# Kernel optimization log

Measured on AMD Instinct MI355X. Metric: run time of the kernel, lower is better.

Reference implementation:

```python
import jax, jax.numpy as jnp
import numpy as np

VOCAB, D_MODEL, N_EXPERTS, TOP_K = 32000, 768, 8, 2
D_FF = 4 * D_MODEL
BATCH, SEQ = 2, 2048


def setup_inputs() -> dict:
    key = jax.random.key(0)
    ks = jax.random.split(key, 6)
    s = 0.02
    return {
        "x": jax.random.randint(ks[0], (BATCH, SEQ), 0, VOCAB),
        "emb": jax.random.normal(ks[1], (VOCAB, D_MODEL), jnp.float32) * s,
        "gate_w": jax.random.normal(ks[2], (D_MODEL, N_EXPERTS), jnp.float32) * s,
        "gate_b": jnp.zeros((N_EXPERTS,), jnp.float32),
        "exp_w": jax.random.normal(ks[3], (N_EXPERTS, D_MODEL, D_FF), jnp.float32) * s,
        "exp_b": jnp.zeros((N_EXPERTS, D_FF), jnp.float32),
        "head_w": jax.random.normal(ks[4], (D_FF, VOCAB), jnp.float32) * s,
        "head_b": jnp.zeros((VOCAB,), jnp.float32),
    }


def reference(x, emb, gate_w, gate_b, exp_w, exp_b, head_w, head_b):
    B, S = x.shape
    h = emb[x]                                   # [B,S,D] embedding gather
    t = h.reshape(B * S, -1)                     # [T,D] token view
    logits = t @ gate_w + gate_b                 # [T,E] router
    topv, topi = jax.lax.top_k(logits, TOP_K)    # top-2 routing
    w = jax.nn.softmax(topv, axis=-1)            # renormalized gate weights
    T = t.shape[0]
    gates = jnp.zeros_like(logits).at[jnp.arange(T)[:, None], topi].set(w)  # [T,E]
    # expert FFN: Linear(d_model -> 4*d_model) + ReLU, dense over experts
    exp_out = jax.nn.relu(jnp.einsum('td,edf->tef', t, exp_w) + exp_b)      # [T,E,F]
    moe = jnp.einsum('te,tef->tf', gates, exp_out)                          # combine
    out = moe @ head_w + head_b                  # [T,V]
    return out.reshape(B, S, -1)
```

## Files before the change

### kernel.cpp

```cpp
#include <hip/hip_runtime.h>

typedef unsigned short u16;
typedef __attribute__((ext_vector_type(8))) short short8;
typedef __attribute__((ext_vector_type(4))) float f32x4;

#define T_TOKENS 4096
#define DMODEL   768
#define DFF      3072
#define NEXP     8
#define NVOCAB   32000

__device__ __forceinline__ u16 f2bf(float f) {
  unsigned u = __float_as_uint(f);
  u += 0x7FFFu + ((u >> 16) & 1u);
  return (u16)(u >> 16);
}
__device__ __forceinline__ float bf2f(u16 b) {
  return __uint_as_float(((unsigned)b) << 16);
}

__device__ __forceinline__ void async_load16(const void* g, void* lds) {
  __builtin_amdgcn_global_load_lds((const __attribute__((address_space(1))) void*)g,
                                   (__attribute__((address_space(3))) void*)lds, 16, 0, 0);
}

#define SBAR() __builtin_amdgcn_s_barrier()
#define VMCNT(n) asm volatile("s_waitcnt vmcnt(" #n ")")

__global__ __launch_bounds__(256) void k_embed_router(
    const int* __restrict__ x, const float* __restrict__ emb,
    const float* __restrict__ gw, const float* __restrict__ gb,
    u16* __restrict__ tbf, int* __restrict__ counts,
    int* __restrict__ tlist, float* __restrict__ wlist)
{
  __shared__ float partial[4][NEXP];
  const int t = blockIdx.x;
  const int tok = x[t];
  const float* er = emb + (size_t)tok * DMODEL;
  float p[NEXP];
#pragma unroll
  for (int e = 0; e < NEXP; ++e) p[e] = 0.f;
#pragma unroll
  for (int i = 0; i < 3; ++i) {
    const int d = threadIdx.x + i * 256;
    const float v = er[d];
    tbf[(size_t)t * DMODEL + d] = f2bf(v);
#pragma unroll
    for (int e = 0; e < NEXP; ++e) p[e] += v * gw[d * NEXP + e];
  }
#pragma unroll
  for (int e = 0; e < NEXP; ++e)
#pragma unroll
    for (int m = 32; m >= 1; m >>= 1) p[e] += __shfl_xor(p[e], m);
  const int lane = threadIdx.x & 63, wv = threadIdx.x >> 6;
  if (lane == 0)
    for (int e = 0; e < NEXP; ++e) partial[wv][e] = p[e];
  __syncthreads();
  if (threadIdx.x == 0) {
    float l[NEXP];
    for (int e = 0; e < NEXP; ++e)
      l[e] = partial[0][e] + partial[1][e] + partial[2][e] + partial[3][e] + gb[e];
    int i0 = 0;
    for (int e = 1; e < NEXP; ++e) if (l[e] > l[i0]) i0 = e;
    int i1 = -1;
    for (int e = 0; e < NEXP; ++e) { if (e == i0) continue; if (i1 < 0 || l[e] > l[i1]) i1 = e; }
    const float w0 = 1.f / (1.f + expf(l[i1] - l[i0]));
    int p0 = atomicAdd(&counts[0 * NEXP + i0], 1);
    tlist[(0 * NEXP + i0) * T_TOKENS + p0] = t;
    wlist[(0 * NEXP + i0) * T_TOKENS + p0] = w0;
    int p1 = atomicAdd(&counts[1 * NEXP + i1], 1);
    tlist[(1 * NEXP + i1) * T_TOKENS + p1] = t;
    wlist[(1 * NEXP + i1) * T_TOKENS + p1] = 1.f - w0;
  }
}

__global__ __launch_bounds__(256) void k_transpose_cvt(
    const float* __restrict__ src, u16* __restrict__ dst, int R, int C)
{
  __shared__ float tile[32][33];
  const float* s = src + (size_t)blockIdx.z * R * C;
  u16* d = dst + (size_t)blockIdx.z * R * C;
  const int tx = threadIdx.x & 31, ty = threadIdx.x >> 5;
  const int c = blockIdx.x * 32 + tx;
#pragma unroll
  for (int i = 0; i < 4; ++i) {
    const int r = blockIdx.y * 32 + ty + i * 8;
    tile[ty + i * 8][tx] = s[(size_t)r * C + c];
  }
  __syncthreads();
  const int rr = blockIdx.y * 32 + tx;
#pragma unroll
  for (int i = 0; i < 4; ++i) {
    const int cc = blockIdx.x * 32 + ty + i * 8;
    d[(size_t)cc * R + rr] = f2bf(tile[tx][ty + i * 8]);
  }
}

template <int SLOT1>
__global__ __launch_bounds__(256) void k_ffn_slot(
    const u16* __restrict__ tbf, const u16* __restrict__ BT,
    const float* __restrict__ eb, const int* __restrict__ counts,
    const int* __restrict__ tlist, const float* __restrict__ wlist,
    u16* __restrict__ moe)
{
  const int e = blockIdx.z;
  const int cnt = counts[SLOT1 * NEXP + e];
  const int mb = blockIdx.y;
  if (mb * 128 >= cnt) return;
  const int base = (SLOT1 * NEXP + e) * T_TOKENS + mb * 128;
  const int lim = cnt - mb * 128;

  __shared__ u16 aT[128 * 64];
  __shared__ u16 bT[128 * 64];
  const int tid = threadIdx.x;
  const int wave = tid >> 6, lane = tid & 63;
  const int wm = wave >> 1, wn = wave & 1;
  const int kg = lane >> 4, fr = lane & 15;
  const int n0 = blockIdx.x * 128;
  const u16* Be = BT + (size_t)e * DFF * DMODEL;

  int tokm[4];
#pragma unroll
  for (int it = 0; it < 4; ++it) {
    const int m = (it * 256 + tid) >> 3;
    tokm[it] = tlist[base + (m < lim ? m : lim - 1)];
  }

  f32x4 acc[4][4] = {};
  for (int ks = 0; ks < DMODEL / 64; ++ks) {
    __syncthreads();
    const int kb = ks * 64;
#pragma unroll
    for (int it = 0; it < 4; ++it) {
      const int c = it * 256 + tid;
      const int m = c >> 3;
      const int slot = (c & 7) ^ (m & 7);
      async_load16(tbf + (size_t)tokm[it] * DMODEL + kb + slot * 8,
                   &aT[(it * 256 + wave * 64) * 8]);
      async_load16(Be + (size_t)(n0 + m) * DMODEL + kb + slot * 8,
                   &bT[(it * 256 + wave * 64) * 8]);
    }
    __syncthreads();
#pragma unroll
    for (int kk = 0; kk < 2; ++kk) {
      short8 af[4], bf[4];
#pragma unroll
      for (int i = 0; i < 4; ++i) {
        const int am = wm * 64 + i * 16 + fr;
        const int kc = kk * 4 + kg;
        af[i] = *(const short8*)&aT[(am * 8 + (kc ^ (am & 7))) * 8];
        const int bn = wn * 64 + i * 16 + fr;
        bf[i] = *(const short8*)&bT[(bn * 8 + (kc ^ (bn & 7))) * 8];
      }
#pragma unroll
      for (int i = 0; i < 4; ++i)
#pragma unroll
        for (int j = 0; j < 4; ++j)
          acc[i][j] = __builtin_amdgcn_mfma_f32_16x16x32_bf16(af[i], bf[j], acc[i][j], 0, 0, 0);
    }
  }

  int trow[4][4]; float wrow[4][4];
#pragma unroll
  for (int i = 0; i < 4; ++i)
#pragma unroll
    for (int r = 0; r < 4; ++r) {
      const int row = wm * 64 + i * 16 + kg * 4 + r;
      if (row < lim) { trow[i][r] = tlist[base + row]; wrow[i][r] = wlist[base + row]; }
      else trow[i][r] = -1;
    }
#pragma unroll
  for (int j = 0; j < 4; ++j) {
    const int col = n0 + wn * 64 + j * 16 + fr;
    const float b = eb[e * DFF + col];
#pragma unroll
    for (int i = 0; i < 4; ++i)
#pragma unroll
      for (int r = 0; r < 4; ++r) {
        if (trow[i][r] < 0) continue;
        float v = acc[i][j][r] + b;
        v = v > 0.f ? v : 0.f;
        v *= wrow[i][r];
        u16* dst = &moe[(size_t)trow[i][r] * DFF + col];
        if (SLOT1) v += bf2f(*dst);
        *dst = f2bf(v);
      }
  }
}

__device__ __forceinline__ short8 frag(const u16* buf, int row, int kc) {
  return *(const short8*)(buf + (row * 8 + (kc ^ (row & 7))) * 8);
}

__global__ __launch_bounds__(512, 2) void k_head(
    const u16* __restrict__ A, const u16* __restrict__ BT,
    const float* __restrict__ bias, float* __restrict__ C)
{
  __shared__ u16 aL[2][256 * 64];
  __shared__ u16 bL[2][256 * 64];
  const int tid = threadIdx.x;
  const int lane = tid & 63, wave = tid >> 6;
  const int wm = wave >> 2, wn = wave & 3;
  const int kg = lane >> 4, fr = lane & 15;
  const int wg = (int)blockIdx.x;
  const int swz = (wg & 7) * 250 + (wg >> 3);
  const int m0 = (swz & 15) * 256;
  const int n0 = (swz >> 4) * 256;
  const int K = DFF, NT = K / 64;

  size_t gAo[2], gBo[2]; int lAo[2], lBo[2];
#pragma unroll
  for (int i = 0; i < 2; ++i) {
    const int c = i * 512 + tid, rl = c >> 3, s = c & 7;
    const int rA = (rl & 63) + ((rl >> 6) << 7);
    const int gsA = s ^ (rA & 7);
    gAo[i] = (size_t)(m0 + rA) * K + gsA * 8;
    lAo[i] = rA * 64 + s * 8;
    const int rB = (rl & 31) + ((rl >> 5) << 6);
    const int gsB = s ^ (rB & 7);
    gBo[i] = (size_t)(n0 + rB) * K + gsB * 8;
    lBo[i] = rB * 64 + s * 8;
  }
  auto stageA = [&](int kb, u16* buf, int h) {
#pragma unroll
    for (int i = 0; i < 2; ++i)
      async_load16(A + gAo[i] + (size_t)(h * 64) * K + kb, buf + lAo[i] + h * 4096);
  };
  auto stageB = [&](int kb, u16* buf, int h) {
#pragma unroll
    for (int i = 0; i < 2; ++i)
      async_load16(BT + gBo[i] + (size_t)(h * 32) * K + kb, buf + lBo[i] + h * 2048);
  };

  f32x4 acc[8][4] = {};
  short8 af0[4][2], af1[4][2], bfl[2][2], bfh[2][2];

  stageA(0, aL[0], 0); stageA(0, aL[0], 1);
  stageB(0, bL[0], 0); stageB(0, bL[0], 1);
  stageA(64, aL[1], 0); stageB(64, bL[1], 0); stageA(64, aL[1], 1);
  VMCNT(6);
  __builtin_amdgcn_sched_barrier(0);
  SBAR();
#pragma unroll
  for (int mi = 0; mi < 4; ++mi)
#pragma unroll
    for (int kk = 0; kk < 2; ++kk)
      af0[mi][kk] = frag(aL[0], wm * 128 + mi * 16 + fr, kk * 4 + kg);
#pragma unroll
  for (int ni = 0; ni < 2; ++ni)
#pragma unroll
    for (int kk = 0; kk < 2; ++kk)
      bfl[ni][kk] = frag(bL[0], wn * 64 + ni * 16 + fr, kk * 4 + kg);

  for (int t = 0; t < NT; ++t) {
    const int cur = t & 1;
    const u16* a_ = aL[cur];
    const u16* b_ = bL[cur];
    u16* aw = aL[cur];
    u16* bw = bL[cur];
    const u16* an = aL[cur ^ 1];
    const u16* bn = bL[cur ^ 1];
    const int kb1 = (t + 1) * 64, kb2 = (t + 2) * 64;

#pragma unroll
    for (int ni = 0; ni < 2; ++ni)
#pragma unroll
      for (int kk = 0; kk < 2; ++kk)
        bfh[ni][kk] = frag(b_, wn * 64 + 32 + ni * 16 + fr, kk * 4 + kg);
    if (t + 1 < NT) stageB(kb1, bL[cur ^ 1], 1);
    __builtin_amdgcn_s_setprio(1);
#pragma unroll
    for (int mi = 0; mi < 4; ++mi)
#pragma unroll
      for (int ni = 0; ni < 2; ++ni)
#pragma unroll
        for (int kk = 0; kk < 2; ++kk)
          acc[mi][ni] = __builtin_amdgcn_mfma_f32_16x16x32_bf16(af0[mi][kk], bfl[ni][kk], acc[mi][ni], 0, 0, 0);
    __builtin_amdgcn_s_setprio(0);
    SBAR();

#pragma unroll
    for (int mi = 0; mi < 4; ++mi)
#pragma unroll
      for (int kk = 0; kk < 2; ++kk)
        af1[mi][kk] = frag(a_, wm * 128 + 64 + mi * 16 + fr, kk * 4 + kg);
    if (t + 2 < NT) stageA(kb2, aw, 0);
    __builtin_amdgcn_s_setprio(1);
#pragma unroll
    for (int mi = 0; mi < 4; ++mi)
#pragma unroll
      for (int ni = 0; ni < 2; ++ni)
#pragma unroll
        for (int kk = 0; kk < 2; ++kk)
          acc[mi][ni + 2] = __builtin_amdgcn_mfma_f32_16x16x32_bf16(af0[mi][kk], bfh[ni][kk], acc[mi][ni + 2], 0, 0, 0);
    __builtin_amdgcn_s_setprio(0);
    if (t < NT - 2) { VMCNT(8); } else if (t == NT - 2) { VMCNT(6); }
    __builtin_amdgcn_sched_barrier(0);
    SBAR();

    if (t + 1 < NT) {
#pragma unroll
      for (int mi = 0; mi < 4; ++mi)
#pragma unroll
        for (int kk = 0; kk < 2; ++kk)
          af0[mi][kk] = frag(an, wm * 128 + mi * 16 + fr, kk * 4 + kg);
    }
    if (t + 2 < NT) stageB(kb2, bw, 0);
    __builtin_amdgcn_s_setprio(1);
#pragma unroll
    for (int mi = 0; mi < 4; ++mi)
#pragma unroll
      for (int ni = 0; ni < 2; ++ni)
#pragma unroll
        for (int kk = 0; kk < 2; ++kk)
          acc[mi + 4][ni] = __builtin_amdgcn_mfma_f32_16x16x32_bf16(af1[mi][kk], bfl[ni][kk], acc[mi + 4][ni], 0, 0, 0);
    __builtin_amdgcn_s_setprio(0);
    if (t < NT - 2) { VMCNT(8); } else if (t == NT - 2) { VMCNT(4); }
    __builtin_amdgcn_sched_barrier(0);
    SBAR();

    if (t + 1 < NT) {
#pragma unroll
      for (int ni = 0; ni < 2; ++ni)
#pragma unroll
        for (int kk = 0; kk < 2; ++kk)
          bfl[ni][kk] = frag(bn, wn * 64 + ni * 16 + fr, kk * 4 + kg);
    }
    if (t + 2 < NT) stageA(kb2, aw, 1);
    __builtin_amdgcn_s_setprio(1);
#pragma unroll
    for (int mi = 0; mi < 4; ++mi)
#pragma unroll
      for (int ni = 0; ni < 2; ++ni)
#pragma unroll
        for (int kk = 0; kk < 2; ++kk)
          acc[mi + 4][ni + 2] = __builtin_amdgcn_mfma_f32_16x16x32_bf16(af1[mi][kk], bfh[ni][kk], acc[mi + 4][ni + 2], 0, 0, 0);
    __builtin_amdgcn_s_setprio(0);
    if (t < NT - 2) { VMCNT(6); } else if (t == NT - 2) { VMCNT(0); }
    __builtin_amdgcn_sched_barrier(0);
    SBAR();
  }

#pragma unroll
  for (int ni = 0; ni < 4; ++ni) {
    const int col = n0 + wn * 64 + ni * 16 + fr;
    const float b = bias[col];
#pragma unroll
    for (int mi = 0; mi < 8; ++mi) {
      const int row = m0 + wm * 128 + (mi >> 2) * 64 + (mi & 3) * 16 + kg * 4;
#pragma unroll
      for (int r = 0; r < 4; ++r)
        __builtin_nontemporal_store(acc[mi][ni][r] + b,
                                    &C[(size_t)(row + r) * NVOCAB + col]);
    }
  }
}

extern "C" void kernel_launch(void* const* d_in, const int* in_sizes, int n_in,
                              void* d_out, int out_size, void* d_ws, size_t ws_size,
                              hipStream_t stream) {
  const int*   x     = (const int*)d_in[0];
  const float* emb   = (const float*)d_in[1];
  const float* gw    = (const float*)d_in[2];
  const float* gb    = (const float*)d_in[3];
  const float* expw  = (const float*)d_in[4];
  const float* expb  = (const float*)d_in[5];
  const float* headw = (const float*)d_in[6];
  const float* headb = (const float*)d_in[7];
  float* out = (float*)d_out;

  char* ws = (char*)d_ws;
  size_t off = 0;
  auto alloc = [&](size_t bytes) { size_t r = off; off += (bytes + 255) & ~(size_t)255; return r; };
  u16*   tbf    = (u16*)(ws + alloc((size_t)T_TOKENS * DMODEL * 2));
  int*   counts = (int*)(ws + alloc(2 * NEXP * 4));
  int*   tlist  = (int*)(ws + alloc((size_t)2 * NEXP * T_TOKENS * 4));
  float* wlist  = (float*)(ws + alloc((size_t)2 * NEXP * T_TOKENS * 4));
  u16*   expwT  = (u16*)(ws + alloc((size_t)NEXP * DFF * DMODEL * 2));
  u16*   headwT = (u16*)(ws + alloc((size_t)NVOCAB * DFF * 2));
  u16*   moe    = (u16*)(ws + alloc((size_t)T_TOKENS * DFF * 2));

  hipMemsetAsync(counts, 0, 2 * NEXP * 4, stream);
  k_embed_router<<<T_TOKENS, 256, 0, stream>>>(x, emb, gw, gb, tbf, counts, tlist, wlist);
  k_transpose_cvt<<<dim3(DFF / 32, DMODEL / 32, NEXP), 256, 0, stream>>>(expw, expwT, DMODEL, DFF);
  k_transpose_cvt<<<dim3(NVOCAB / 32, DFF / 32, 1), 256, 0, stream>>>(headw, headwT, DFF, NVOCAB);
  k_ffn_slot<0><<<dim3(DFF / 128, T_TOKENS / 128, NEXP), 256, 0, stream>>>(
      tbf, expwT, expb, counts, tlist, wlist, moe);
  k_ffn_slot<1><<<dim3(DFF / 128, T_TOKENS / 128, NEXP), 256, 0, stream>>>(
      tbf, expwT, expb, counts, tlist, wlist, moe);
  k_head<<<(T_TOKENS / 256) * (NVOCAB / 256), 512, 0, stream>>>(moe, headwT, headb, out);
}
```

Measured before the change: 1.246 ms.

## Shrink head GEMM tile to 128x128 with 4 waves and re-pipeline LDS staging

The vocabulary head GEMM moves from 256x256 tiles with 8 waves and 512 threads to 128x128 tiles with 4 waves and 256 threads, each wave computing 64x64. The K-loop is restructured into four phases per 64-wide K step, with explicit lgkmcnt waits and new vmcnt thresholds. The grid grows fourfold, which aims to improve load balance and occupancy. In exchange, reuse of A and B tiles per loaded byte drops, so global and L2 traffic rises.

Result: slower. 1.883 ms (+51.2%).

```diff
diff --git a/kernel.cpp b/kernel.cpp
--- a/kernel.cpp
+++ b/kernel.cpp
@@ -26,6 +26,8 @@
 
 #define SBAR() __builtin_amdgcn_s_barrier()
 #define VMCNT(n) asm volatile("s_waitcnt vmcnt(" #n ")")
+#define LGKM(n)  asm volatile("s_waitcnt lgkmcnt(" #n ")")
+#define SCHEDB() __builtin_amdgcn_sched_barrier(0)
 
 __global__ __launch_bounds__(256) void k_embed_router(
     const int* __restrict__ x, const float* __restrict__ emb,
@@ -192,165 +194,147 @@
   return *(const short8*)(buf + (row * 8 + (kc ^ (row & 7))) * 8);
 }
 
-__global__ __launch_bounds__(512, 2) void k_head(
+__global__ __launch_bounds__(256) void k_head(
     const u16* __restrict__ A, const u16* __restrict__ BT,
     const float* __restrict__ bias, float* __restrict__ C)
 {
-  __shared__ u16 aL[2][256 * 64];
-  __shared__ u16 bL[2][256 * 64];
+  __shared__ u16 aL[2][128 * 64];
+  __shared__ u16 bL[2][128 * 64];
   const int tid = threadIdx.x;
   const int lane = tid & 63, wave = tid >> 6;
-  const int wm = wave >> 2, wn = wave & 3;
+  const int wm = wave >> 1, wn = wave & 1;
   const int kg = lane >> 4, fr = lane & 15;
   const int wg = (int)blockIdx.x;
-  const int swz = (wg & 7) * 250 + (wg >> 3);
-  const int m0 = (swz & 15) * 256;
-  const int n0 = (swz >> 4) * 256;
+  const int swz = (wg & 7) * 1000 + (wg >> 3);
+  const int m0 = (swz & 31) * 128;
+  const int n0 = (swz >> 5) * 128;
   const int K = DFF, NT = K / 64;
 
-  size_t gAo[2], gBo[2]; int lAo[2], lBo[2];
+  size_t gAo[2], gBo[2]; int lOf[2];
 #pragma unroll
   for (int i = 0; i < 2; ++i) {
-    const int c = i * 512 + tid, rl = c >> 3, s = c & 7;
-    const int rA = (rl & 63) + ((rl >> 6) << 7);
-    const int gsA = s ^ (rA & 7);
-    gAo[i] = (size_t)(m0 + rA) * K + gsA * 8;
-    lAo[i] = rA * 64 + s * 8;
-    const int rB = (rl & 31) + ((rl >> 5) << 6);
-    const int gsB = s ^ (rB & 7);
-    gBo[i] = (size_t)(n0 + rB) * K + gsB * 8;
-    lBo[i] = rB * 64 + s * 8;
+    const int c = i * 256 + tid, rl = c >> 3, s = c & 7;
+    const int gs = s ^ (rl & 7);
+    gAo[i] = (size_t)(m0 + rl) * K + gs * 8;
+    gBo[i] = (size_t)(n0 + rl) * K + gs * 8;
+    lOf[i] = (rl * 8 + s) * 8;
   }
   auto stageA = [&](int kb, u16* buf, int h) {
 #pragma unroll
     for (int i = 0; i < 2; ++i)
-      async_load16(A + gAo[i] + (size_t)(h * 64) * K + kb, buf + lAo[i] + h * 4096);
+      async_load16(A + gAo[i] + (size_t)(h * 64) * K + kb, buf + lOf[i] + h * 4096);
   };
   auto stageB = [&](int kb, u16* buf, int h) {
 #pragma unroll
     for (int i = 0; i < 2; ++i)
-      async_load16(BT + gBo[i] + (size_t)(h * 32) * K + kb, buf + lBo[i] + h * 2048);
+      async_load16(BT + gBo[i] + (size_t)(h * 64) * K + kb, buf + lOf[i] + h * 4096);
   };
 
-  f32x4 acc[8][4] = {};
-  short8 af0[4][2], af1[4][2], bfl[2][2], bfh[2][2];
+  f32x4 acc[4][4] = {};
+  short8 af[4][2], bf[4][2];
 
   stageA(0, aL[0], 0); stageA(0, aL[0], 1);
   stageB(0, bL[0], 0); stageB(0, bL[0], 1);
-  stageA(64, aL[1], 0); stageB(64, bL[1], 0); stageA(64, aL[1], 1);
+  stageA(64, aL[1], 0); stageA(64, aL[1], 1); stageB(64, bL[1], 0);
   VMCNT(6);
-  __builtin_amdgcn_sched_barrier(0);
+  SCHEDB();
   SBAR();
 #pragma unroll
   for (int mi = 0; mi < 4; ++mi)
-#pragma unroll
-    for (int kk = 0; kk < 2; ++kk)
-      af0[mi][kk] = frag(aL[0], wm * 128 + mi * 16 + fr, kk * 4 + kg);
-#pragma unroll
-  for (int ni = 0; ni < 2; ++ni)
-#pragma unroll
-    for (int kk = 0; kk < 2; ++kk)
-      bfl[ni][kk] = frag(bL[0], wn * 64 + ni * 16 + fr, kk * 4 + kg);
+    af[mi][0] = frag(aL[0], wm * 64 + mi * 16 + fr, kg);
+#pragma unroll
+  for (int nj = 0; nj < 2; ++nj)
+    bf[nj][0] = frag(bL[0], wn * 64 + nj * 16 + fr, kg);
 
   for (int t = 0; t < NT; ++t) {
     const int cur = t & 1;
     const u16* a_ = aL[cur];
     const u16* b_ = bL[cur];
+    const u16* an = aL[cur ^ 1];
+    const u16* bn = bL[cur ^ 1];
     u16* aw = aL[cur];
     u16* bw = bL[cur];
-    const u16* an = aL[cur ^ 1];
-    const u16* bn = bL[cur ^ 1];
+    u16* bwn = bL[cur ^ 1];
     const int kb1 = (t + 1) * 64, kb2 = (t + 2) * 64;
 
 #pragma unroll
-    for (int ni = 0; ni < 2; ++ni)
-#pragma unroll
-      for (int kk = 0; kk < 2; ++kk)
-        bfh[ni][kk] = frag(b_, wn * 64 + 32 + ni * 16 + fr, kk * 4 + kg);
-    if (t + 1 < NT) stageB(kb1, bL[cur ^ 1], 1);
+    for (int nj = 2; nj < 4; ++nj)
+      bf[nj][0] = frag(b_, wn * 64 + nj * 16 + fr, kg);
+    if (t + 1 < NT) stageB(kb1, bwn, 1);
     __builtin_amdgcn_s_setprio(1);
 #pragma unroll
     for (int mi = 0; mi < 4; ++mi)
 #pragma unroll
-      for (int ni = 0; ni < 2; ++ni)
-#pragma unroll
-        for (int kk = 0; kk < 2; ++kk)
-          acc[mi][ni] = __builtin_amdgcn_mfma_f32_16x16x32_bf16(af0[mi][kk], bfl[ni][kk], acc[mi][ni], 0, 0, 0);
+      for (int nj = 0; nj < 2; ++nj)
+        acc[mi][nj] = __builtin_amdgcn_mfma_f32_16x16x32_bf16(af[mi][0], bf[nj][0], acc[mi][nj], 0, 0, 0);
     __builtin_amdgcn_s_setprio(0);
     SBAR();
 
 #pragma unroll
     for (int mi = 0; mi < 4; ++mi)
-#pragma unroll
-      for (int kk = 0; kk < 2; ++kk)
-        af1[mi][kk] = frag(a_, wm * 128 + 64 + mi * 16 + fr, kk * 4 + kg);
+      af[mi][1] = frag(a_, wm * 64 + mi * 16 + fr, 4 + kg);
+#pragma unroll
+    for (int nj = 0; nj < 2; ++nj)
+      bf[nj][1] = frag(b_, wn * 64 + nj * 16 + fr, 4 + kg);
+    __builtin_amdgcn_s_setprio(1);
+#pragma unroll
+    for (int mi = 0; mi < 4; ++mi)
+#pragma unroll
+      for (int nj = 2; nj < 4; ++nj)
+        acc[mi][nj] = __builtin_amdgcn_mfma_f32_16x16x32_bf16(af[mi][0], bf[nj][0], acc[mi][nj], 0, 0, 0);
+    __builtin_amdgcn_s_setprio(0);
+    SBAR();
+
+#pragma unroll
+    for (int nj = 2; nj < 4; ++nj)
+      bf[nj][1] = frag(b_, wn * 64 + nj * 16 + fr, 4 + kg);
+    LGKM(2);
+    SCHEDB();
     if (t + 2 < NT) stageA(kb2, aw, 0);
     __builtin_amdgcn_s_setprio(1);
 #pragma unroll
     for (int mi = 0; mi < 4; ++mi)
 #pragma unroll
-      for (int ni = 0; ni < 2; ++ni)
-#pragma unroll
-        for (int kk = 0; kk < 2; ++kk)
-          acc[mi][ni + 2] = __builtin_amdgcn_mfma_f32_16x16x32_bf16(af0[mi][kk], bfh[ni][kk], acc[mi][ni + 2], 0, 0, 0);
+      for (int nj = 0; nj < 2; ++nj)
+        acc[mi][nj] = __builtin_amdgcn_mfma_f32_16x16x32_bf16(af[mi][1], bf[nj][1], acc[mi][nj], 0, 0, 0);
     __builtin_amdgcn_s_setprio(0);
-    if (t < NT - 2) { VMCNT(8); } else if (t == NT - 2) { VMCNT(6); }
-    __builtin_amdgcn_sched_barrier(0);
+    if (t < NT - 2) { VMCNT(2); } else { VMCNT(0); }
+    SCHEDB();
     SBAR();
 
     if (t + 1 < NT) {
 #pragma unroll
       for (int mi = 0; mi < 4; ++mi)
-#pragma unroll
-        for (int kk = 0; kk < 2; ++kk)
-          af0[mi][kk] = frag(an, wm * 128 + mi * 16 + fr, kk * 4 + kg);
-    }
-    if (t + 2 < NT) stageB(kb2, bw, 0);
+        af[mi][0] = frag(an, wm * 64 + mi * 16 + fr, kg);
+#pragma unroll
+      for (int nj = 0; nj < 2; ++nj)
+        bf[nj][0] = frag(bn, wn * 64 + nj * 16 + fr, kg);
+      LGKM(6);
+    } else {
+      LGKM(0);
+    }
+    SCHEDB();
+    if (t + 2 < NT) { stageA(kb2, aw, 1); stageB(kb2, bw, 0); }
     __builtin_amdgcn_s_setprio(1);
 #pragma unroll
     for (int mi = 0; mi < 4; ++mi)
 #pragma unroll
-      for (int ni = 0; ni < 2; ++ni)
-#pragma unroll
-        for (int kk = 0; kk < 2; ++kk)
-          acc[mi + 4][ni] = __builtin_amdgcn_mfma_f32_16x16x32_bf16(af1[mi][kk], bfl[ni][kk], acc[mi + 4][ni], 0, 0, 0);
+      for (int nj = 2; nj < 4; ++nj)
+        acc[mi][nj] = __builtin_amdgcn_mfma_f32_16x16x32_bf16(af[mi][1], bf[nj][1], acc[mi][nj], 0, 0, 0);
     __builtin_amdgcn_s_setprio(0);
-    if (t < NT - 2) { VMCNT(8); } else if (t == NT - 2) { VMCNT(4); }
-    __builtin_amdgcn_sched_barrier(0);
     SBAR();
-
-    if (t + 1 < NT) {
-#pragma unroll
-      for (int ni = 0; ni < 2; ++ni)
-#pragma unroll
-        for (int kk = 0; kk < 2; ++kk)
-          bfl[ni][kk] = frag(bn, wn * 64 + ni * 16 + fr, kk * 4 + kg);
-    }
-    if (t + 2 < NT) stageA(kb2, aw, 1);
-    __builtin_amdgcn_s_setprio(1);
-#pragma unroll
-    for (int mi = 0; mi < 4; ++mi)
-#pragma unroll
-      for (int ni = 0; ni < 2; ++ni)
-#pragma unroll
-        for (int kk = 0; kk < 2; ++kk)
-          acc[mi + 4][ni + 2] = __builtin_amdgcn_mfma_f32_16x16x32_bf16(af1[mi][kk], bfh[ni][kk], acc[mi + 4][ni + 2], 0, 0, 0);
-    __builtin_amdgcn_s_setprio(0);
-    if (t < NT - 2) { VMCNT(6); } else if (t == NT - 2) { VMCNT(0); }
-    __builtin_amdgcn_sched_barrier(0);
-    SBAR();
-  }
-
-#pragma unroll
-  for (int ni = 0; ni < 4; ++ni) {
-    const int col = n0 + wn * 64 + ni * 16 + fr;
+  }
+
+#pragma unroll
+  for (int nj = 0; nj < 4; ++nj) {
+    const int col = n0 + wn * 64 + nj * 16 + fr;
     const float b = bias[col];
 #pragma unroll
-    for (int mi = 0; mi < 8; ++mi) {
-      const int row = m0 + wm * 128 + (mi >> 2) * 64 + (mi & 3) * 16 + kg * 4;
+    for (int mi = 0; mi < 4; ++mi) {
+      const int row = m0 + wm * 64 + mi * 16 + kg * 4;
 #pragma unroll
       for (int r = 0; r < 4; ++r)
-        __builtin_nontemporal_store(acc[mi][ni][r] + b,
+        __builtin_nontemporal_store(acc[mi][nj][r] + b,
                                     &C[(size_t)(row + r) * NVOCAB + col]);
     }
   }
@@ -388,5 +372,5 @@
       tbf, expwT, expb, counts, tlist, wlist, moe);
   k_ffn_slot<1><<<dim3(DFF / 128, T_TOKENS / 128, NEXP), 256, 0, stream>>>(
       tbf, expwT, expb, counts, tlist, wlist, moe);
-  k_head<<<(T_TOKENS / 256) * (NVOCAB / 256), 512, 0, stream>>>(moe, headwT, headb, out);
-}
+  k_head<<<(T_TOKENS / 128) * (NVOCAB / 128), 256, 0, stream>>>(moe, headwT, headb, out);
+}
```

## Restructure head GEMM main loop into two phases with merged A fragment buffer

Applied to the files above, without the earlier changes.

Reworks the software-pipelined MFMA loop of the vocab-head GEMM from four quarter-tile phases with four barriers per k-step into two half-tile phases with two barriers. A single A-fragment register set is reused and all B fragments (low and high halves) are loaded together. Async global-to-LDS staging is reordered, with vmcnt waits retuned. This cuts barrier and wait overhead per iteration and frees registers, at the risk of less load/compute overlap or an incorrect wait count causing races.

Measured after the change: 1.181 ms. 1.05x faster.

```diff
diff --git a/kernel.cpp b/kernel.cpp
--- a/kernel.cpp
+++ b/kernel.cpp
@@ -26,6 +26,7 @@
 
 #define SBAR() __builtin_amdgcn_s_barrier()
 #define VMCNT(n) asm volatile("s_waitcnt vmcnt(" #n ")")
+#define SCHEDB() __builtin_amdgcn_sched_barrier(0)
 
 __global__ __launch_bounds__(256) void k_embed_router(
     const int* __restrict__ x, const float* __restrict__ emb,
@@ -233,24 +234,26 @@
   };
 
   f32x4 acc[8][4] = {};
-  short8 af0[4][2], af1[4][2], bfl[2][2], bfh[2][2];
+  short8 af[4][2], bfl[2][2], bfh[2][2];
 
   stageA(0, aL[0], 0); stageA(0, aL[0], 1);
   stageB(0, bL[0], 0); stageB(0, bL[0], 1);
-  stageA(64, aL[1], 0); stageB(64, bL[1], 0); stageA(64, aL[1], 1);
+  stageA(64, aL[1], 0); stageB(64, bL[1], 0); stageB(64, bL[1], 1);
   VMCNT(6);
-  __builtin_amdgcn_sched_barrier(0);
+  SCHEDB();
   SBAR();
 #pragma unroll
   for (int mi = 0; mi < 4; ++mi)
 #pragma unroll
     for (int kk = 0; kk < 2; ++kk)
-      af0[mi][kk] = frag(aL[0], wm * 128 + mi * 16 + fr, kk * 4 + kg);
+      af[mi][kk] = frag(aL[0], wm * 128 + mi * 16 + fr, kk * 4 + kg);
 #pragma unroll
   for (int ni = 0; ni < 2; ++ni)
 #pragma unroll
-    for (int kk = 0; kk < 2; ++kk)
+    for (int kk = 0; kk < 2; ++kk) {
       bfl[ni][kk] = frag(bL[0], wn * 64 + ni * 16 + fr, kk * 4 + kg);
+      bfh[ni][kk] = frag(bL[0], wn * 64 + 32 + ni * 16 + fr, kk * 4 + kg);
+    }
 
   for (int t = 0; t < NT; ++t) {
     const int cur = t & 1;
@@ -258,86 +261,58 @@
     const u16* b_ = bL[cur];
     u16* aw = aL[cur];
     u16* bw = bL[cur];
-    const u16* an = aL[cur ^ 1];
+    u16* an = aL[cur ^ 1];
     const u16* bn = bL[cur ^ 1];
     const int kb1 = (t + 1) * 64, kb2 = (t + 2) * 64;
 
-#pragma unroll
-    for (int ni = 0; ni < 2; ++ni)
+    if (t + 1 < NT) stageA(kb1, an, 1);
+    __builtin_amdgcn_s_setprio(1);
+#pragma unroll
+    for (int mi = 0; mi < 4; ++mi)
+#pragma unroll
+      for (int ni = 0; ni < 2; ++ni)
+#pragma unroll
+        for (int kk = 0; kk < 2; ++kk) {
+          acc[mi][ni]     = __builtin_amdgcn_mfma_f32_16x16x32_bf16(af[mi][kk], bfl[ni][kk], acc[mi][ni], 0, 0, 0);
+          acc[mi][ni + 2] = __builtin_amdgcn_mfma_f32_16x16x32_bf16(af[mi][kk], bfh[ni][kk], acc[mi][ni + 2], 0, 0, 0);
+        }
+    __builtin_amdgcn_s_setprio(0);
+#pragma unroll
+    for (int mi = 0; mi < 4; ++mi)
 #pragma unroll
       for (int kk = 0; kk < 2; ++kk)
-        bfh[ni][kk] = frag(b_, wn * 64 + 32 + ni * 16 + fr, kk * 4 + kg);
-    if (t + 1 < NT) stageB(kb1, bL[cur ^ 1], 1);
+        af[mi][kk] = frag(a_, wm * 128 + 64 + mi * 16 + fr, kk * 4 + kg);
+    if (t + 1 < NT) { VMCNT(2); SCHEDB(); }
+    SBAR();
+
+    if (t + 2 < NT) { stageA(kb2, aw, 0); stageB(kb2, bw, 0); stageB(kb2, bw, 1); }
     __builtin_amdgcn_s_setprio(1);
 #pragma unroll
     for (int mi = 0; mi < 4; ++mi)
 #pragma unroll
       for (int ni = 0; ni < 2; ++ni)
 #pragma unroll
+        for (int kk = 0; kk < 2; ++kk) {
+          acc[mi + 4][ni]     = __builtin_amdgcn_mfma_f32_16x16x32_bf16(af[mi][kk], bfl[ni][kk], acc[mi + 4][ni], 0, 0, 0);
+          acc[mi + 4][ni + 2] = __builtin_amdgcn_mfma_f32_16x16x32_bf16(af[mi][kk], bfh[ni][kk], acc[mi + 4][ni + 2], 0, 0, 0);
+        }
+    __builtin_amdgcn_s_setprio(0);
+    if (t + 1 < NT) {
+#pragma unroll
+      for (int mi = 0; mi < 4; ++mi)
+#pragma unroll
         for (int kk = 0; kk < 2; ++kk)
-          acc[mi][ni] = __builtin_amdgcn_mfma_f32_16x16x32_bf16(af0[mi][kk], bfl[ni][kk], acc[mi][ni], 0, 0, 0);
-    __builtin_amdgcn_s_setprio(0);
-    SBAR();
-
-#pragma unroll
-    for (int mi = 0; mi < 4; ++mi)
-#pragma unroll
-      for (int kk = 0; kk < 2; ++kk)
-        af1[mi][kk] = frag(a_, wm * 128 + 64 + mi * 16 + fr, kk * 4 + kg);
-    if (t + 2 < NT) stageA(kb2, aw, 0);
-    __builtin_amdgcn_s_setprio(1);
-#pragma unroll
-    for (int mi = 0; mi < 4; ++mi)
+          af[mi][kk] = frag(an, wm * 128 + mi * 16 + fr, kk * 4 + kg);
 #pragma unroll
       for (int ni = 0; ni < 2; ++ni)
 #pragma unroll
-        for (int kk = 0; kk < 2; ++kk)
-          acc[mi][ni + 2] = __builtin_amdgcn_mfma_f32_16x16x32_bf16(af0[mi][kk], bfh[ni][kk], acc[mi][ni + 2], 0, 0, 0);
-    __builtin_amdgcn_s_setprio(0);
-    if (t < NT - 2) { VMCNT(8); } else if (t == NT - 2) { VMCNT(6); }
-    __builtin_amdgcn_sched_barrier(0);
-    SBAR();
-
-    if (t + 1 < NT) {
-#pragma unroll
-      for (int mi = 0; mi < 4; ++mi)
-#pragma unroll
-        for (int kk = 0; kk < 2; ++kk)
-          af0[mi][kk] = frag(an, wm * 128 + mi * 16 + fr, kk * 4 + kg);
-    }
-    if (t + 2 < NT) stageB(kb2, bw, 0);
-    __builtin_amdgcn_s_setprio(1);
-#pragma unroll
-    for (int mi = 0; mi < 4; ++mi)
-#pragma unroll
-      for (int ni = 0; ni < 2; ++ni)
-#pragma unroll
-        for (int kk = 0; kk < 2; ++kk)
-          acc[mi + 4][ni] = __builtin_amdgcn_mfma_f32_16x16x32_bf16(af1[mi][kk], bfl[ni][kk], acc[mi + 4][ni], 0, 0, 0);
-    __builtin_amdgcn_s_setprio(0);
-    if (t < NT - 2) { VMCNT(8); } else if (t == NT - 2) { VMCNT(4); }
-    __builtin_amdgcn_sched_barrier(0);
-    SBAR();
-
-    if (t + 1 < NT) {
-#pragma unroll
-      for (int ni = 0; ni < 2; ++ni)
-#pragma unroll
-        for (int kk = 0; kk < 2; ++kk)
+        for (int kk = 0; kk < 2; ++kk) {
           bfl[ni][kk] = frag(bn, wn * 64 + ni * 16 + fr, kk * 4 + kg);
-    }
-    if (t + 2 < NT) stageA(kb2, aw, 1);
-    __builtin_amdgcn_s_setprio(1);
-#pragma unroll
-    for (int mi = 0; mi < 4; ++mi)
-#pragma unroll
-      for (int ni = 0; ni < 2; ++ni)
-#pragma unroll
-        for (int kk = 0; kk < 2; ++kk)
-          acc[mi + 4][ni + 2] = __builtin_amdgcn_mfma_f32_16x16x32_bf16(af1[mi][kk], bfh[ni][kk], acc[mi + 4][ni + 2], 0, 0, 0);
-    __builtin_amdgcn_s_setprio(0);
-    if (t < NT - 2) { VMCNT(6); } else if (t == NT - 2) { VMCNT(0); }
-    __builtin_amdgcn_sched_barrier(0);
+          bfh[ni][kk] = frag(bn, wn * 64 + 32 + ni * 16 + fr, kk * 4 + kg);
+        }
+      if (t + 2 < NT) { VMCNT(6); } else { VMCNT(0); }
+      SCHEDB();
+    }
     SBAR();
   }
 
```
